# Optimization experiments

Measured on AMD Instinct MI355X. Metric: run time of the kernel, lower is better.

Reference implementation:

```python
import jax, jax.numpy as jnp
import numpy as np

B, T, C = 16, 1024, 768
H = 12
D = C // H  # 64 head dim


def setup_inputs() -> dict:
    key = jax.random.key(0)
    k1, k2, k3, k4, k5 = jax.random.split(key, 5)
    s = 0.02
    return {
        "x": jax.random.normal(k1, (B, T, C), dtype=jnp.float32),
        "w_attn": jax.random.normal(k2, (C, 3 * C), dtype=jnp.float32) * s,
        "b_attn": jax.random.normal(k3, (3 * C,), dtype=jnp.float32) * s,
        "w_proj": jax.random.normal(k4, (C, C), dtype=jnp.float32) * s,
        "b_proj": jax.random.normal(k5, (C,), dtype=jnp.float32) * s,
    }


def reference(x, w_attn, b_attn, w_proj, b_proj):
    Bc, Tc, Cc = x.shape
    qkv = x @ w_attn + b_attn  # [B,T,3C]
    q, k, v = jnp.split(qkv, 3, axis=-1)
    # [B,T,C] -> [B,H,T,D]
    q = q.reshape(Bc, Tc, H, D).transpose(0, 2, 1, 3)
    k = k.reshape(Bc, Tc, H, D).transpose(0, 2, 1, 3)
    v = v.reshape(Bc, Tc, H, D).transpose(0, 2, 1, 3)
    scale = 1.0 / np.sqrt(D).astype(np.float32)
    atn = jnp.einsum("bhqd,bhkd->bhqk", q, k) * scale
    causal = jnp.tril(jnp.ones((Tc, Tc), dtype=bool))
    atn = jnp.where(causal[None, None], atn, -jnp.inf)
    atn = jax.nn.softmax(atn, axis=-1)
    y = jnp.einsum("bhqk,bhkd->bhqd", atn, v)
    y = y.transpose(0, 2, 1, 3).reshape(Bc, Tc, Cc)
    return y @ w_proj + b_proj
```

## Files before the change

kernel.cpp:

```cpp
#include <hip/hip_runtime.h>
#include <hip/hip_bf16.h>

typedef __attribute__((ext_vector_type(4))) float f32x4;
typedef __attribute__((ext_vector_type(8))) short s16x8;
typedef __attribute__((ext_vector_type(4))) short s16x4;

#define AS1 __attribute__((address_space(1)))
#define AS3 __attribute__((address_space(3)))

__device__ __forceinline__ short f2bf(float f) {
    union { float f; unsigned u; } a; a.f = f;
    unsigned r = a.u + 0x7fff + ((a.u >> 16) & 1);
    return (short)(r >> 16);
}

__device__ __forceinline__ unsigned pk_bf16(float a, float b) {
    unsigned r;
    asm("v_cvt_pk_bf16_f32 %0, %1, %2" : "=v"(r) : "v"(a), "v"(b));
    return r;
}


__global__ __launch_bounds__(256) void convert_f32_bf16(const float* __restrict__ in,
                                                        short* __restrict__ out, int n4) {
    int i = blockIdx.x * 256 + threadIdx.x;
    if (i < n4) {
        f32x4 v = *(const f32x4*)(in + (long)i * 4);
        s16x4 o;
        o.x = f2bf(v.x); o.y = f2bf(v.y); o.z = f2bf(v.z); o.w = f2bf(v.w);
        *(s16x4*)(out + (long)i * 4) = o;
    }
}

__global__ __launch_bounds__(256) void transpose_w(const float* __restrict__ src,
                                                   short* __restrict__ dst, int K, int N) {
    __shared__ short t[64][65];
    int k0 = blockIdx.x * 64, n0 = blockIdx.y * 64;
    int tid = threadIdx.x;
    for (int i = tid; i < 64 * 64; i += 256) {
        int r = i >> 6, c = i & 63;
        t[r][c] = f2bf(src[(long)(k0 + r) * N + n0 + c]);
    }
    __syncthreads();
    for (int i = tid; i < 64 * 64; i += 256) {
        int r = i >> 6, c = i & 63;
        dst[(long)(n0 + r) * K + k0 + c] = t[c][r];
    }
}

__global__ __launch_bounds__(256) void transpose_vp(const short* __restrict__ vp,
                                                    short* __restrict__ vt) {
    __shared__ short t[64][72];
    int t0 = blockIdx.x * 64;
    int g = blockIdx.y;
    int tid = threadIdx.x;
#pragma unroll
    for (int i = 0; i < 2; ++i) {
        int j = tid + i * 256;
        int r = j >> 3, c = j & 7;
        s16x8 v = *(const s16x8*)(vp + ((long)g * 1024 + t0 + r) * 64 + c * 8);
#pragma unroll
        for (int e = 0; e < 8; ++e) t[c * 8 + e][r] = v[e];
    }
    __syncthreads();
#pragma unroll
    for (int i = 0; i < 2; ++i) {
        int j = tid + i * 256;
        int r = j >> 3, c = j & 7;
        *(s16x8*)(vt + ((long)g * 64 + r) * 1024 + t0 + c * 8) = *(const s16x8*)&t[r][c * 8];
    }
}


template <int MODE>
__global__ __launch_bounds__(256) void gemm_bt(const short* __restrict__ A,
                                               const short* __restrict__ BT,
                                               const float* __restrict__ bias,
                                               float* __restrict__ outF,
                                               short* __restrict__ q_,
                                               short* __restrict__ k_,
                                               short* __restrict__ v_,
                                               int M, int N, int K) {
    __shared__ short lA[2 * 64 * 64];
    __shared__ short lB[2 * 64 * 64];
    int tid = threadIdx.x;
    int lane = tid & 63, w = tid >> 6;
    int wr = w >> 1, wc = w & 1;
    int lo = lane & 15, hi = lane >> 4;

    int bid = blockIdx.x;
    int swz = (bid & 7) * ((int)gridDim.x >> 3) + (bid >> 3);
    int NX = N >> 7;
    int bx = swz % NX, by = swz / NX;
    int m0 = by * 128, n0 = bx * 128;

    f32x4 acc[4][4];
#pragma unroll
    for (int i = 0; i < 4; ++i)
#pragma unroll
        for (int j = 0; j < 4; ++j) acc[i][j] = (f32x4){0.f, 0.f, 0.f, 0.f};

    const short* Abase = A + (long)m0 * K;
    const short* Bbase = BT + (long)n0 * K;

    int lr = lane >> 3;
    int cc = (lane & 7) ^ lr;
    int growoff = cc >> 2;
    int gcol = (cc & 3) * 8;

    int srlo = lo >> 1;
    int rpar = (lo & 1) << 2;

    for (int k0 = 0; k0 < K; k0 += 64) {
        __syncthreads();
#pragma unroll
        for (int kk = 0; kk < 2; ++kk)
#pragma unroll
            for (int j = 0; j < 2; ++j) {
                int sr = w * 16 + j * 8 + lr;
                long grow = (long)(sr * 2 + growoff);
                const short* ga = Abase + grow * K + k0 + kk * 32 + gcol;
                const short* gb = Bbase + grow * K + k0 + kk * 32 + gcol;
                short* da = lA + kk * 4096 + (w * 16 + j * 8) * 64;
                short* db = lB + kk * 4096 + (w * 16 + j * 8) * 64;
                __builtin_amdgcn_global_load_lds((const AS1 void*)ga, (AS3 void*)da, 16, 0, 0);
                __builtin_amdgcn_global_load_lds((const AS1 void*)gb, (AS3 void*)db, 16, 0, 0);
            }
        __syncthreads();

#pragma unroll
        for (int kk = 0; kk < 2; ++kk) {
            s16x8 a[4], b[4];
#pragma unroll
            for (int mi = 0; mi < 4; ++mi)
                a[mi] = *(const s16x8*)(lA + kk * 4096 + (wr * 32 + mi * 8 + srlo) * 64 +
                                        ((rpar + hi) ^ srlo) * 8);
#pragma unroll
            for (int ni = 0; ni < 4; ++ni)
                b[ni] = *(const s16x8*)(lB + kk * 4096 + (wc * 32 + ni * 8 + srlo) * 64 +
                                        ((rpar + hi) ^ srlo) * 8);
#pragma unroll
            for (int mi = 0; mi < 4; ++mi)
#pragma unroll
                for (int ni = 0; ni < 4; ++ni)
                    acc[mi][ni] = __builtin_amdgcn_mfma_f32_16x16x32_bf16(a[mi], b[ni], acc[mi][ni], 0, 0, 0);
        }
    }

    float bs[4];
#pragma unroll
    for (int ni = 0; ni < 4; ++ni) bs[ni] = bias[n0 + wc * 64 + ni * 16 + lo];

    if (MODE == 1) {
        int blk = (n0 + wc * 64) >> 6;
        int part = (blk >= 24) ? 2 : (blk >= 12 ? 1 : 0);
        int hh = blk - part * 12;
        short* dst = (part == 0) ? q_ : (part == 1) ? k_ : v_;
        float scl = (part == 0) ? 0.180336880f : 1.0f;
        int bidx = m0 >> 10;
        int trow0 = (m0 & 1023) + wr * 64;
        long gb_ = ((long)(bidx * 12 + hh)) << 16;
#pragma unroll
        for (int mi = 0; mi < 4; ++mi)
#pragma unroll
            for (int ni = 0; ni < 4; ++ni)
#pragma unroll
                for (int r = 0; r < 4; ++r) {
                    int trow = trow0 + mi * 16 + hi * 4 + r;
                    float v = (acc[mi][ni][r] + bs[ni]) * scl;
                    dst[gb_ + (long)trow * 64 + ni * 16 + lo] = f2bf(v);
                }
    } else {
#pragma unroll
        for (int mi = 0; mi < 4; ++mi)
#pragma unroll
            for (int ni = 0; ni < 4; ++ni)
#pragma unroll
                for (int r = 0; r < 4; ++r) {
                    int gm = m0 + wr * 64 + mi * 16 + hi * 4 + r;
                    int gn = n0 + wc * 64 + ni * 16 + lo;
                    outF[(long)gm * N + gn] = acc[mi][ni][r] + bs[ni];
                }
    }
}


__device__ __forceinline__ void attn_tile(const short* __restrict__ Kb,
                                          const short* __restrict__ Vb,
                                          int kv0, int qb0, bool diag,
                                          s16x8 bq0, s16x8 bq1,
                                          f32x4 (&ov)[4], float& mrun, float& lrun,
                                          int lo, int hi, int hi2, int sA, int sB,
                                          int sl0, int sl1) {
    f32x4 s[4];
#pragma unroll
    for (int n = 0; n < 4; ++n) {
        const short* kr = Kb + (n * 16 + lo) * 64;
        s16x8 kf0 = *(const s16x8*)(kr + sl0);
        s16x8 kf1 = *(const s16x8*)(kr + sl1);
        f32x4 t = (f32x4){0.f, 0.f, 0.f, 0.f};
        t = __builtin_amdgcn_mfma_f32_16x16x32_bf16(kf0, bq0, t, 0, 0, 0);
        t = __builtin_amdgcn_mfma_f32_16x16x32_bf16(kf1, bq1, t, 0, 0, 0);
        s[n] = t;
    }
    s16x8 av0[4], av1[4];
#pragma unroll
    for (int nd = 0; nd < 4; ++nd) {
        const short* vr = Vb + (nd * 16 + lo) * 64;
        av0[nd] = *(const s16x8*)(vr + sl0);
        av1[nd] = *(const s16x8*)(vr + sl1);
    }

    int qglob = qb0 + lo;
    if (diag) {
#pragma unroll
        for (int n = 0; n < 4; ++n)
#pragma unroll
            for (int r = 0; r < 4; ++r)
                if (kv0 + n * 16 + hi * 4 + r > qglob) s[n][r] = -3.0e38f;
    }
    float mx = s[0][0];
#pragma unroll
    for (int n = 0; n < 4; ++n)
#pragma unroll
        for (int r = 0; r < 4; ++r) mx = fmaxf(mx, s[n][r]);
    mx = fmaxf(mx, __shfl_xor(mx, 16));
    mx = fmaxf(mx, __shfl_xor(mx, 32));
    float mn = fmaxf(mrun, mx);
    float alpha = exp2f(mrun - mn);
    mrun = mn;
    float rs = 0.f;
#pragma unroll
    for (int n = 0; n < 4; ++n)
#pragma unroll
        for (int r = 0; r < 4; ++r) {
            float p = exp2f(s[n][r] - mn);
            s[n][r] = p;
            rs += p;
        }
    rs += __shfl_xor(rs, 16);
    rs += __shfl_xor(rs, 32);
    lrun = lrun * alpha + rs;
#pragma unroll
    for (int nd = 0; nd < 4; ++nd)
#pragma unroll
        for (int r = 0; r < 4; ++r) ov[nd][r] *= alpha;

    unsigned W[4][2];
#pragma unroll
    for (int n = 0; n < 4; ++n) {
        W[n][0] = pk_bf16(s[n][0], s[n][1]);
        W[n][1] = pk_bf16(s[n][2], s[n][3]);
    }
    s16x8 ap[2];
#pragma unroll
    for (int kc = 0; kc < 2; ++kc) {
        unsigned a0 = __shfl(W[kc * 2][0], sA), b0 = __shfl(W[kc * 2 + 1][0], sA);
        unsigned a1 = __shfl(W[kc * 2][1], sA), b1 = __shfl(W[kc * 2 + 1][1], sA);
        unsigned a2 = __shfl(W[kc * 2][0], sB), b2 = __shfl(W[kc * 2 + 1][0], sB);
        unsigned a3 = __shfl(W[kc * 2][1], sB), b3 = __shfl(W[kc * 2 + 1][1], sB);
        union { unsigned u[4]; s16x8 v; } cv;
        cv.u[0] = hi2 ? b0 : a0;
        cv.u[1] = hi2 ? b1 : a1;
        cv.u[2] = hi2 ? b2 : a2;
        cv.u[3] = hi2 ? b3 : a3;
        ap[kc] = cv.v;
    }
#pragma unroll
    for (int nd = 0; nd < 4; ++nd) {
        ov[nd] = __builtin_amdgcn_mfma_f32_16x16x32_bf16(av0[nd], ap[0], ov[nd], 0, 0, 0);
        ov[nd] = __builtin_amdgcn_mfma_f32_16x16x32_bf16(av1[nd], ap[1], ov[nd], 0, 0, 0);
    }
}

__device__ __forceinline__ void store_out(const f32x4 (&ov)[4], float lrun,
                                          long rowbase, int qb0, int h,
                                          int lo, int hi, short* __restrict__ y) {
    float inv = 1.0f / lrun;
    long row = (rowbase + qb0 + lo) * 768 + h * 64;
#pragma unroll
    for (int nd = 0; nd < 4; ++nd)
#pragma unroll
        for (int j2 = 0; j2 < 2; ++j2) {
            unsigned pv = pk_bf16(ov[nd][2 * j2] * inv, ov[nd][2 * j2 + 1] * inv);
            *(unsigned*)(y + row + nd * 16 + hi * 4 + 2 * j2) = pv;
        }
}

__global__ __launch_bounds__(256) void flash_attn7(const short* __restrict__ qpk,
                                                   const short* __restrict__ kpk,
                                                   const short* __restrict__ vtg,
                                                   short* __restrict__ y) {
    __shared__ short Kb[2][4096];
    __shared__ short Vb[2][4096];

    int d = blockIdx.x;
    int qp = d / 192, g = d % 192;
    int h = g % 12, b = g / 12;
    int tid = threadIdx.x, lane = tid & 63, w = tid >> 6;
    int lo = lane & 15, hi = lane >> 4, hi2 = hi >> 1;
    long rowbase = (long)b * 1024;
    const short* kb_g = kpk + (long)g * 65536;
    const short* vt_g = vtg + (long)g * 65536;
    int sA = ((hi & 1) * 2) * 16 + lo, sB = sA + 16;

    int rl = lane >> 3;
    int cs8 = (((lane & 7) ^ rl)) * 8;
    int r0 = w * 8 + rl;
    int sl0 = (hi ^ (lo & 7)) * 8;
    int sl1 = ((hi + 4) ^ (lo & 7)) * 8;

    int qbA = qp * 64 + w * 16;
    int qbB = (15 - qp) * 64 + w * 16;

    f32x4 ov[4];
    float mrun = -3.0e38f, lrun = 0.f;
#pragma unroll
    for (int nd = 0; nd < 4; ++nd) ov[nd] = (f32x4){0.f, 0.f, 0.f, 0.f};
    s16x8 bq0, bq1;
    {
        const short* qrow = qpk + ((long)g * 1024 + qbA + lo) * 64;
        bq0 = *(const s16x8*)(qrow + hi * 8);
        bq1 = *(const s16x8*)(qrow + 32 + hi * 8);
    }

#define STAGE(kv0_, buf_)                                                                    \
    do {                                                                                     \
        _Pragma("unroll")                                                                    \
        for (int i_ = 0; i_ < 2; ++i_) {                                                     \
            int r_ = i_ * 32 + r0;                                                           \
            __builtin_amdgcn_global_load_lds(                                                \
                (const AS1 void*)(kb_g + (long)((kv0_) + r_) * 64 + cs8),                    \
                (AS3 void*)(Kb[buf_] + (i_ * 32 + w * 8) * 64), 16, 0, 0);                   \
            __builtin_amdgcn_global_load_lds(                                                \
                (const AS1 void*)(vt_g + (long)r_ * 1024 + (kv0_) + cs8),                    \
                (AS3 void*)(Vb[buf_] + (i_ * 32 + w * 8) * 64), 16, 0, 0);                   \
        }                                                                                    \
    } while (0)

    STAGE(0, 0);
    __syncthreads();

    int cur = 0;
    for (int u = 0; u < 17; ++u) {
        int nu = u + 1;
        if (nu < 17) {
            int nkv0 = (nu <= qp) ? nu * 64 : (nu - qp - 1) * 64;
            STAGE(nkv0, cur ^ 1);
        }
        bool phaseA = (u <= qp);
        int kv0 = phaseA ? u * 64 : (u - qp - 1) * 64;
        int qb0 = phaseA ? qbA : qbB;
        bool diag = phaseA ? (u == qp) : (u == 16);
        attn_tile(Kb[cur], Vb[cur], kv0, qb0, diag, bq0, bq1, ov, mrun, lrun,
                  lo, hi, hi2, sA, sB, sl0, sl1);
        if (phaseA && u == qp) {
            store_out(ov, lrun, rowbase, qbA, h, lo, hi, y);
            const short* qrow = qpk + ((long)g * 1024 + qbB + lo) * 64;
            bq0 = *(const s16x8*)(qrow + hi * 8);
            bq1 = *(const s16x8*)(qrow + 32 + hi * 8);
#pragma unroll
            for (int nd = 0; nd < 4; ++nd) ov[nd] = (f32x4){0.f, 0.f, 0.f, 0.f};
            mrun = -3.0e38f; lrun = 0.f;
        }
        __syncthreads();
        cur ^= 1;
    }
    store_out(ov, lrun, rowbase, qbB, h, lo, hi, y);
#undef STAGE
}


extern "C" void kernel_launch(void* const* d_in, const int* in_sizes, int n_in,
                              void* d_out, int out_size, void* d_ws, size_t ws_size,
                              hipStream_t stream) {
    const float* x      = (const float*)d_in[0];
    const float* w_attn = (const float*)d_in[1];
    const float* b_attn = (const float*)d_in[2];
    const float* w_proj = (const float*)d_in[3];
    const float* b_proj = (const float*)d_in[4];

    char* ws = (char*)d_ws;
    short* x_bf = (short*)ws;
    short* qpk  = (short*)(ws + 25165824);
    short* kpk  = (short*)(ws + 50331648);
    short* vpk  = (short*)(ws + 75497472);
    short* yb   = (short*)(ws + 100663296);
    short* waT  = (short*)(ws + 125829120);
    short* wpT  = (short*)(ws + 129368064);
    short* vt   = x_bf;

    convert_f32_bf16<<<dim3(12288), dim3(256), 0, stream>>>(x, x_bf, 3145728);
    transpose_w<<<dim3(12, 36), dim3(256), 0, stream>>>(w_attn, waT, 768, 2304);
    transpose_w<<<dim3(12, 12), dim3(256), 0, stream>>>(w_proj, wpT, 768, 768);
    gemm_bt<1><<<dim3(2304), dim3(256), 0, stream>>>(x_bf, waT, b_attn,
                                                     (float*)nullptr, qpk, kpk, vpk,
                                                     16384, 2304, 768);
    transpose_vp<<<dim3(16, 192), dim3(256), 0, stream>>>(vpk, vt);
    flash_attn7<<<dim3(1536), dim3(256), 0, stream>>>(qpk, kpk, vt, yb);
    gemm_bt<0><<<dim3(768), dim3(256), 0, stream>>>(yb, wpT, b_proj,
                                                    (float*)d_out, (short*)nullptr,
                                                    (short*)nullptr, (short*)nullptr,
                                                    16384, 768, 768);
}
```

Before: 214.8 us.

## Split attention tile into QK-softmax and PV phases with single-buffered V staging

Splits the attention tile into a QK/softmax phase and a PV accumulation phase separated by a barrier. V becomes single-buffered: it is loaded after PV finishes and overlaps the next tile's QK/softmax, while K stays double-buffered. s_setprio is raised around the MFMA sections to favour matrix work across waves. This halves V's LDS footprint, which may allow more resident blocks, but it adds a barrier per iteration and exposes V load latency if QK/softmax is too short to hide it.

```diff
diff --git a/kernel.cpp b/kernel.cpp
--- a/kernel.cpp
+++ b/kernel.cpp
@@ -185,17 +185,18 @@
 }
 
 
-__device__ __forceinline__ void attn_tile(const short* __restrict__ Kb,
-                                          const short* __restrict__ Vb,
-                                          int kv0, int qb0, bool diag,
-                                          s16x8 bq0, s16x8 bq1,
-                                          f32x4 (&ov)[4], float& mrun, float& lrun,
-                                          int lo, int hi, int hi2, int sA, int sB,
-                                          int sl0, int sl1) {
+__device__ __forceinline__ void qk_softmax(const short* __restrict__ Kb_,
+                                           int kv0, int qb0, bool diag,
+                                           s16x8 bq0, s16x8 bq1,
+                                           f32x4 (&ov)[4], float& mrun, float& lrun,
+                                           s16x8 (&ap)[2],
+                                           int lo, int hi, int hi2, int sA, int sB,
+                                           int sl0, int sl1) {
     f32x4 s[4];
+    __builtin_amdgcn_s_setprio(1);
 #pragma unroll
     for (int n = 0; n < 4; ++n) {
-        const short* kr = Kb + (n * 16 + lo) * 64;
+        const short* kr = Kb_ + (n * 16 + lo) * 64;
         s16x8 kf0 = *(const s16x8*)(kr + sl0);
         s16x8 kf1 = *(const s16x8*)(kr + sl1);
         f32x4 t = (f32x4){0.f, 0.f, 0.f, 0.f};
@@ -203,13 +204,7 @@
         t = __builtin_amdgcn_mfma_f32_16x16x32_bf16(kf1, bq1, t, 0, 0, 0);
         s[n] = t;
     }
-    s16x8 av0[4], av1[4];
-#pragma unroll
-    for (int nd = 0; nd < 4; ++nd) {
-        const short* vr = Vb + (nd * 16 + lo) * 64;
-        av0[nd] = *(const s16x8*)(vr + sl0);
-        av1[nd] = *(const s16x8*)(vr + sl1);
-    }
+    __builtin_amdgcn_s_setprio(0);
 
     int qglob = qb0 + lo;
     if (diag) {
@@ -252,7 +247,6 @@
         W[n][0] = pk_bf16(s[n][0], s[n][1]);
         W[n][1] = pk_bf16(s[n][2], s[n][3]);
     }
-    s16x8 ap[2];
 #pragma unroll
     for (int kc = 0; kc < 2; ++kc) {
         unsigned a0 = __shfl(W[kc * 2][0], sA), b0 = __shfl(W[kc * 2 + 1][0], sA);
@@ -266,11 +260,21 @@
         cv.u[3] = hi2 ? b3 : a3;
         ap[kc] = cv.v;
     }
+}
+
+__device__ __forceinline__ void pv_accum(const short* __restrict__ Vb_,
+                                         const s16x8 (&ap)[2], f32x4 (&ov)[4],
+                                         int lo, int sl0, int sl1) {
+    __builtin_amdgcn_s_setprio(1);
 #pragma unroll
     for (int nd = 0; nd < 4; ++nd) {
-        ov[nd] = __builtin_amdgcn_mfma_f32_16x16x32_bf16(av0[nd], ap[0], ov[nd], 0, 0, 0);
-        ov[nd] = __builtin_amdgcn_mfma_f32_16x16x32_bf16(av1[nd], ap[1], ov[nd], 0, 0, 0);
-    }
+        const short* vr = Vb_ + (nd * 16 + lo) * 64;
+        s16x8 av0 = *(const s16x8*)(vr + sl0);
+        s16x8 av1 = *(const s16x8*)(vr + sl1);
+        ov[nd] = __builtin_amdgcn_mfma_f32_16x16x32_bf16(av0, ap[0], ov[nd], 0, 0, 0);
+        ov[nd] = __builtin_amdgcn_mfma_f32_16x16x32_bf16(av1, ap[1], ov[nd], 0, 0, 0);
+    }
+    __builtin_amdgcn_s_setprio(0);
 }
 
 __device__ __forceinline__ void store_out(const f32x4 (&ov)[4], float lrun,
@@ -287,12 +291,12 @@
         }
 }
 
-__global__ __launch_bounds__(256) void flash_attn7(const short* __restrict__ qpk,
+__global__ __launch_bounds__(256) void flash_attn8(const short* __restrict__ qpk,
                                                    const short* __restrict__ kpk,
                                                    const short* __restrict__ vtg,
                                                    short* __restrict__ y) {
     __shared__ short Kb[2][4096];
-    __shared__ short Vb[2][4096];
+    __shared__ short Vb[4096];
 
     int d = blockIdx.x;
     int qp = d / 192, g = d % 192;
@@ -324,7 +328,7 @@
         bq1 = *(const s16x8*)(qrow + 32 + hi * 8);
     }
 
-#define STAGE(kv0_, buf_)                                                                    \
+#define STAGE_K(kv0_, buf_)                                                                  \
     do {                                                                                     \
         _Pragma("unroll")                                                                    \
         for (int i_ = 0; i_ < 2; ++i_) {                                                     \
@@ -332,28 +336,44 @@
             __builtin_amdgcn_global_load_lds(                                                \
                 (const AS1 void*)(kb_g + (long)((kv0_) + r_) * 64 + cs8),                    \
                 (AS3 void*)(Kb[buf_] + (i_ * 32 + w * 8) * 64), 16, 0, 0);                   \
+        }                                                                                    \
+    } while (0)
+
+#define STAGE_V(kv0_)                                                                        \
+    do {                                                                                     \
+        _Pragma("unroll")                                                                    \
+        for (int i_ = 0; i_ < 2; ++i_) {                                                     \
+            int r_ = i_ * 32 + r0;                                                           \
             __builtin_amdgcn_global_load_lds(                                                \
                 (const AS1 void*)(vt_g + (long)r_ * 1024 + (kv0_) + cs8),                    \
-                (AS3 void*)(Vb[buf_] + (i_ * 32 + w * 8) * 64), 16, 0, 0);                   \
+                (AS3 void*)(Vb + (i_ * 32 + w * 8) * 64), 16, 0, 0);                         \
         }                                                                                    \
     } while (0)
 
-    STAGE(0, 0);
+    STAGE_K(0, 0);
+    STAGE_V(0);
     __syncthreads();
 
     int cur = 0;
     for (int u = 0; u < 17; ++u) {
         int nu = u + 1;
-        if (nu < 17) {
-            int nkv0 = (nu <= qp) ? nu * 64 : (nu - qp - 1) * 64;
-            STAGE(nkv0, cur ^ 1);
-        }
+        int nkv0 = (nu <= qp) ? nu * 64 : (nu - qp - 1) * 64;
+        if (nu < 17) STAGE_K(nkv0, cur ^ 1);
+
         bool phaseA = (u <= qp);
         int kv0 = phaseA ? u * 64 : (u - qp - 1) * 64;
         int qb0 = phaseA ? qbA : qbB;
         bool diag = phaseA ? (u == qp) : (u == 16);
-        attn_tile(Kb[cur], Vb[cur], kv0, qb0, diag, bq0, bq1, ov, mrun, lrun,
-                  lo, hi, hi2, sA, sB, sl0, sl1);
+
+        s16x8 ap[2];
+        qk_softmax(Kb[cur], kv0, qb0, diag, bq0, bq1, ov, mrun, lrun, ap,
+                   lo, hi, hi2, sA, sB, sl0, sl1);
+
+        __syncthreads();
+        __builtin_amdgcn_sched_barrier(0);
+
+        pv_accum(Vb, ap, ov, lo, sl0, sl1);
+
         if (phaseA && u == qp) {
             store_out(ov, lrun, rowbase, qbA, h, lo, hi, y);
             const short* qrow = qpk + ((long)g * 1024 + qbB + lo) * 64;
@@ -363,11 +383,15 @@
             for (int nd = 0; nd < 4; ++nd) ov[nd] = (f32x4){0.f, 0.f, 0.f, 0.f};
             mrun = -3.0e38f; lrun = 0.f;
         }
-        __syncthreads();
+
+        __builtin_amdgcn_s_barrier();
+        __builtin_amdgcn_sched_barrier(0);
+        if (nu < 17) STAGE_V(nkv0);
         cur ^= 1;
     }
     store_out(ov, lrun, rowbase, qbB, h, lo, hi, y);
-#undef STAGE
+#undef STAGE_K
+#undef STAGE_V
 }
 
 
@@ -397,7 +421,7 @@
                                                      (float*)nullptr, qpk, kpk, vpk,
                                                      16384, 2304, 768);
     transpose_vp<<<dim3(16, 192), dim3(256), 0, stream>>>(vpk, vt);
-    flash_attn7<<<dim3(1536), dim3(256), 0, stream>>>(qpk, kpk, vt, yb);
+    flash_attn8<<<dim3(1536), dim3(256), 0, stream>>>(qpk, kpk, vt, yb);
     gemm_bt<0><<<dim3(768), dim3(256), 0, stream>>>(yb, wpT, b_proj,
                                                     (float*)d_out, (short*)nullptr,
                                                     (short*)nullptr, (short*)nullptr,
```

After: 211.0 us. About the same (-1.8%).
